# Kernel optimization log

Measured on AMD Instinct MI355X. Metric: run time of the kernel, lower is better.

## Reference

```python
import jax, jax.numpy as jnp
import numpy as np

H = 4096  # grid height
W = 4096  # grid width


def setup_inputs() -> dict:
    key = jax.random.key(0)
    k1, k2 = jax.random.split(key)
    x = jax.random.normal(k1, (H,), dtype=jnp.float32)
    # xavier_uniform with fan_in=3, fan_out=3 => bound = sqrt(6/(3+3)) = 1.0
    bound = float(np.sqrt(6.0 / (3.0 + 3.0)))
    w = jax.random.uniform(k2, (H, W), dtype=jnp.float32, minval=-bound, maxval=bound)
    b = jnp.zeros((H, W), dtype=jnp.float32)
    return {"x": x, "w": w, "b": b}


def _shift_down(a, k):
    # prepend k zero rows / elements along axis 0, drop last k
    pad_shape = (k,) + a.shape[1:]
    return jnp.concatenate([jnp.zeros(pad_shape, a.dtype), a[: a.shape[0] - k]], axis=0)


def reference(x, w, b):
    # The torch module zero-pads w (one row top/bottom) and keeps activation
    # rows 0 and H+1 at zero. The 3-tap stencil a[i-1],a[i],a[i+1] (padded idx)
    # for output row i reduces, in unpadded coords, to:
    #   z[i] = c[i-2]*w[i-2] + c[i-1]*w[i-1] + c[i]*w[i] + b[i]
    # with zero boundary for negative indices.
    Hh, Ww = b.shape
    wm2 = _shift_down(w, 2)  # w[i-2] with zero boundary, (H, W)
    wm1 = _shift_down(w, 1)  # w[i-1]
    # scan across columns (width); carry the activation column (H,)
    xs = (wm2.T, wm1.T, w.T, b.T)  # each (W, H)

    def step(col, ws):
        a2, a1, a0, bj = ws
        z = _shift_down(col, 2) * a2 + _shift_down(col, 1) * a1 + col * a0 + bj
        new = jnp.sin(z)
        return new, None

    final, _ = jax.lax.scan(step, x.reshape(Hh), xs)
    return final.reshape(1, Hh)
```

## Files before the change

### kernel.cpp

```cpp
#include <hip/hip_runtime.h>
#include <math.h>

#define HH 4096
#define WW 4096
#define NB 64
#define U 8
#define NGR (WW / U)
#define GATE 36


__device__ __forceinline__ float f4c(const float4& v, int k) {
    return (k == 0) ? v.x : ((k == 1) ? v.y : ((k == 2) ? v.z : v.w));
}

__device__ __forceinline__ float wave_shr1(float src, float fill) {
    return __int_as_float(__builtin_amdgcn_update_dpp(
        __float_as_int(fill), __float_as_int(src), 0x138, 0xF, 0xF, false));
}

__device__ __forceinline__ float fast_sin(float z) {
    return __builtin_amdgcn_sinf(z * 0.15915494309189535f);
}

#define COLSTEP(COL, M, K)                                                   \
    do {                                                                     \
        float am1 = wave_shr1(a, Hhi[M][K]);                                 \
        float am2 = wave_shr1(am1, Hlo[M][K]);                               \
        const float z = fmaf(am2, f4c(W2v[M][(K) >> 2], (K) & 3),            \
                        fmaf(am1, f4c(W1v[M][(K) >> 2], (K) & 3),            \
                        fmaf(a,   f4c(Wv[M][(K) >> 2],  (K) & 3),            \
                                  f4c(Bv[M][(K) >> 2],  (K) & 3))));         \
        a = fast_sin(z);                                                     \
        if (lane >= 62 && (COL) + 1 < WW) {                                  \
            unsigned long long v =                                           \
                ((unsigned long long)(unsigned)((COL) + 2) << 32) |          \
                (unsigned long long)__float_as_uint(a);                      \
            atomicExch(&hme[(size_t)((COL) + 1) * 2 + (lane - 62)], v);      \
        }                                                                    \
    } while (0)

#define LOADW(M, J)                                                          \
    do {                                                                     \
        const int _j = (J);                                                  \
        Wv[M][0]  = *(const float4*)(wp  + _j);                              \
        Wv[M][1]  = *(const float4*)(wp  + _j + 4);                          \
        W1v[M][0] = *(const float4*)(wp1 + _j);                              \
        W1v[M][1] = *(const float4*)(wp1 + _j + 4);                          \
        W2v[M][0] = *(const float4*)(wp2 + _j);                              \
        W2v[M][1] = *(const float4*)(wp2 + _j + 4);                          \
        Bv[M][0]  = *(const float4*)(bp  + _j);                              \
        Bv[M][1]  = *(const float4*)(bp  + _j + 4);                          \
    } while (0)

#define UNPACKG(GIDX, BUF, SLOT)                                             \
    do {                                                                     \
        const int _jn = (GIDX) * U;                                          \
        if (blk > 0) {                                                       \
            bool myok = (lane >= 16) ||                                      \
                ((unsigned)(Hg[SLOT] >> 32) ==                               \
                 (unsigned)(_jn + (lane >> 1) + 1));                         \
            while (__builtin_expect(!__all(myok), 0)) {                      \
                __builtin_amdgcn_s_sleep(16);                                \
                if (lane < 16)                                               \
                    Hg[SLOT] = atomicOr(&hsrc[(size_t)_jn * 2 + lane], 0ULL);\
                myok = (lane >= 16) ||                                       \
                    ((unsigned)(Hg[SLOT] >> 32) ==                           \
                     (unsigned)(_jn + (lane >> 1) + 1));                     \
            }                                                                \
            float _hv = __uint_as_float((unsigned)(Hg[SLOT] & 0xffffffffu)); \
            _Pragma("unroll")                                                \
            for (int k = 0; k < U; ++k) {                                    \
                Hlo[BUF][k] = __shfl(_hv, 2 * k);                            \
                Hhi[BUF][k] = __shfl(_hv, 2 * k + 1);                        \
            }                                                                \
        }                                                                    \
    } while (0)

#define GROUPBODY(S)                                                         \
    do {                                                                     \
        const int G  = g4 * 4 + (S);                                         \
        const int jb = G * U;                                                \
        if (G + 1 < NGR) UNPACKG(G + 1, ((S) + 1) & 1, ((S) + 1) & 3);       \
        _Pragma("unroll")                                                    \
        for (int k = 0; k < U; ++k) COLSTEP(jb + k, (S) & 1, k);             \
        const int jw = jb + 2 * U;                                           \
        if (jw < WW) LOADW((S) & 1, jw);                                     \
        const int jh = jb + 4 * U;                                           \
        if (jh < WW && blk > 0 && lane < 16)                                 \
            Hg[S] = atomicOr(&hsrc[(size_t)jh * 2 + lane], 0ULL);            \
    } while (0)

__global__ __launch_bounds__(64, 1) void neural_grid_scan(
    const float* __restrict__ x, const float* __restrict__ w,
    const float* __restrict__ bb, float* __restrict__ out,
    unsigned long long* __restrict__ halo)
{
    const int lane = threadIdx.x;
    const int blk  = blockIdx.x;
    const int row  = blk * 64 + lane;
    const int r1 = (row >= 1) ? row - 1 : 0;
    const int r2 = (row >= 2) ? row - 2 : 0;

    const float* wp  = w  + (size_t)row * WW;
    const float* wp1 = w  + (size_t)r1  * WW;
    const float* wp2 = w  + (size_t)r2  * WW;
    const float* bp  = bb + (size_t)row * WW;

    unsigned long long* hme  = halo + (size_t)blk * WW * 2;
    unsigned long long* hsrc = halo + (size_t)(blk - 1) * WW * 2;

    float a = x[row];

    if (lane >= 62) {
        unsigned long long v = (1ULL << 32) | (unsigned long long)__float_as_uint(a);
        atomicExch(&hme[lane - 62], v);
    }

    if (blk > 0 && lane == 0) {
        while ((unsigned)(atomicOr(&hsrc[(size_t)GATE * 2], 0ULL) >> 32)
               != (unsigned)(GATE + 1)) {
            __builtin_amdgcn_s_sleep(8);
        }
    }

    float4 Wv[2][2], W1v[2][2], W2v[2][2], Bv[2][2];
    unsigned long long Hg[4];
    float Hlo[2][U] = {}, Hhi[2][U] = {};

    LOADW(0, 0);
    LOADW(1, U);
    if (blk > 0 && lane < 16) {
        Hg[0] = atomicOr(&hsrc[(size_t)(0 * U) * 2 + lane], 0ULL);
        Hg[1] = atomicOr(&hsrc[(size_t)(1 * U) * 2 + lane], 0ULL);
        Hg[2] = atomicOr(&hsrc[(size_t)(2 * U) * 2 + lane], 0ULL);
        Hg[3] = atomicOr(&hsrc[(size_t)(3 * U) * 2 + lane], 0ULL);
    } else {
        Hg[0] = Hg[1] = Hg[2] = Hg[3] = 0;
    }
    UNPACKG(0, 0, 0);

    for (int g4 = 0; g4 < NGR / 4; ++g4) {
        GROUPBODY(0);
        GROUPBODY(1);
        GROUPBODY(2);
        GROUPBODY(3);
    }

    out[row] = a;
}

extern "C" void kernel_launch(void* const* d_in, const int* in_sizes, int n_in,
                              void* d_out, int out_size, void* d_ws, size_t ws_size,
                              hipStream_t stream) {
    const float* x = (const float*)d_in[0];
    const float* w = (const float*)d_in[1];
    const float* b = (const float*)d_in[2];
    float* out = (float*)d_out;
    unsigned long long* halo = (unsigned long long*)d_ws;
    neural_grid_scan<<<dim3(NB), dim3(64), 0, stream>>>(x, w, b, out, halo);
}
```

Baseline: 904.2 us.

## Process four rows per lane to cut block count and halo chain depth

Each lane now owns four consecutive rows instead of one, so only 16 wavefronts cover the grid instead of 64. This shortens the block-to-block halo dependency chain, and each lane reuses its shared weight rows across its four outputs. In exchange each lane computes four sines per column and loads more weight and bias vectors per group, which raises register pressure and per-wave serial work. The spin-wait sleep is shortened and the start gate is pushed further out.

```diff
diff --git a/kernel.cpp b/kernel.cpp
--- a/kernel.cpp
+++ b/kernel.cpp
@@ -3,10 +3,11 @@
 
 #define HH 4096
 #define WW 4096
-#define NB 64
+#define R 4
+#define NBLK 16
 #define U 8
 #define NGR (WW / U)
-#define GATE 36
+#define GATE 64
 
 
 __device__ __forceinline__ float f4c(const float4& v, int k) {
@@ -24,32 +25,56 @@
 
 #define COLSTEP(COL, M, K)                                                   \
     do {                                                                     \
-        float am1 = wave_shr1(a, Hhi[M][K]);                                 \
-        float am2 = wave_shr1(am1, Hlo[M][K]);                               \
-        const float z = fmaf(am2, f4c(W2v[M][(K) >> 2], (K) & 3),            \
-                        fmaf(am1, f4c(W1v[M][(K) >> 2], (K) & 3),            \
-                        fmaf(a,   f4c(Wv[M][(K) >> 2],  (K) & 3),            \
-                                  f4c(Bv[M][(K) >> 2],  (K) & 3))));         \
-        a = fast_sin(z);                                                     \
-        if (lane >= 62 && (COL) + 1 < WW) {                                  \
-            unsigned long long v =                                           \
-                ((unsigned long long)(unsigned)((COL) + 2) << 32) |          \
-                (unsigned long long)__float_as_uint(a);                      \
-            atomicExch(&hme[(size_t)((COL) + 1) * 2 + (lane - 62)], v);      \
+        const float d1 = wave_shr1(a3, Hhi[M][K]);                           \
+        const float d2 = wave_shr1(a2, Hlo[M][K]);                           \
+        const float w0v = f4c(Wr[M][0][(K) >> 2], (K) & 3);                  \
+        const float w1v = f4c(Wr[M][1][(K) >> 2], (K) & 3);                  \
+        const float w2v = f4c(Wr[M][2][(K) >> 2], (K) & 3);                  \
+        const float w3v = f4c(Wr[M][3][(K) >> 2], (K) & 3);                  \
+        const float w4v = f4c(Wr[M][4][(K) >> 2], (K) & 3);                  \
+        const float w5v = f4c(Wr[M][5][(K) >> 2], (K) & 3);                  \
+        const float n0 = fast_sin(fmaf(d2, w0v, fmaf(d1, w1v,               \
+                          fmaf(a0, w2v, f4c(Br[M][0][(K) >> 2], (K) & 3))))); \
+        const float n1 = fast_sin(fmaf(d1, w1v, fmaf(a0, w2v,               \
+                          fmaf(a1, w3v, f4c(Br[M][1][(K) >> 2], (K) & 3))))); \
+        const float n2 = fast_sin(fmaf(a0, w2v, fmaf(a1, w3v,               \
+                          fmaf(a2, w4v, f4c(Br[M][2][(K) >> 2], (K) & 3))))); \
+        const float n3 = fast_sin(fmaf(a1, w3v, fmaf(a2, w4v,               \
+                          fmaf(a3, w5v, f4c(Br[M][3][(K) >> 2], (K) & 3))))); \
+        a0 = n0; a1 = n1; a2 = n2; a3 = n3;                                  \
+        if (lane == 63 && (COL) + 1 < WW) {                                  \
+            const unsigned long long tg =                                    \
+                ((unsigned long long)(unsigned)((COL) + 2) << 32);           \
+            atomicExch(&hme[(size_t)((COL) + 1) * 2 + 0],                    \
+                       tg | (unsigned long long)__float_as_uint(a2));        \
+            atomicExch(&hme[(size_t)((COL) + 1) * 2 + 1],                    \
+                       tg | (unsigned long long)__float_as_uint(a3));        \
         }                                                                    \
     } while (0)
 
 #define LOADW(M, J)                                                          \
     do {                                                                     \
         const int _j = (J);                                                  \
-        Wv[M][0]  = *(const float4*)(wp  + _j);                              \
-        Wv[M][1]  = *(const float4*)(wp  + _j + 4);                          \
-        W1v[M][0] = *(const float4*)(wp1 + _j);                              \
-        W1v[M][1] = *(const float4*)(wp1 + _j + 4);                          \
-        W2v[M][0] = *(const float4*)(wp2 + _j);                              \
-        W2v[M][1] = *(const float4*)(wp2 + _j + 4);                          \
-        Bv[M][0]  = *(const float4*)(bp  + _j);                              \
-        Bv[M][1]  = *(const float4*)(bp  + _j + 4);                          \
+        Wr[M][0][0] = *(const float4*)(wr0 + _j);                            \
+        Wr[M][0][1] = *(const float4*)(wr0 + _j + 4);                        \
+        Wr[M][1][0] = *(const float4*)(wr1 + _j);                            \
+        Wr[M][1][1] = *(const float4*)(wr1 + _j + 4);                        \
+        Wr[M][2][0] = *(const float4*)(wr2 + _j);                            \
+        Wr[M][2][1] = *(const float4*)(wr2 + _j + 4);                        \
+        Wr[M][3][0] = *(const float4*)(wr3 + _j);                            \
+        Wr[M][3][1] = *(const float4*)(wr3 + _j + 4);                        \
+        Wr[M][4][0] = *(const float4*)(wr4 + _j);                            \
+        Wr[M][4][1] = *(const float4*)(wr4 + _j + 4);                        \
+        Wr[M][5][0] = *(const float4*)(wr5 + _j);                            \
+        Wr[M][5][1] = *(const float4*)(wr5 + _j + 4);                        \
+        Br[M][0][0] = *(const float4*)(br0 + _j);                            \
+        Br[M][0][1] = *(const float4*)(br0 + _j + 4);                        \
+        Br[M][1][0] = *(const float4*)(br1 + _j);                            \
+        Br[M][1][1] = *(const float4*)(br1 + _j + 4);                        \
+        Br[M][2][0] = *(const float4*)(br2 + _j);                            \
+        Br[M][2][1] = *(const float4*)(br2 + _j + 4);                        \
+        Br[M][3][0] = *(const float4*)(br3 + _j);                            \
+        Br[M][3][1] = *(const float4*)(br3 + _j + 4);                        \
     } while (0)
 
 #define UNPACKG(GIDX, BUF, SLOT)                                             \
@@ -60,7 +85,7 @@
                 ((unsigned)(Hg[SLOT] >> 32) ==                               \
                  (unsigned)(_jn + (lane >> 1) + 1));                         \
             while (__builtin_expect(!__all(myok), 0)) {                      \
-                __builtin_amdgcn_s_sleep(16);                                \
+                __builtin_amdgcn_s_sleep(2);                                 \
                 if (lane < 16)                                               \
                     Hg[SLOT] = atomicOr(&hsrc[(size_t)_jn * 2 + lane], 0ULL);\
                 myok = (lane >= 16) ||                                       \
@@ -97,23 +122,28 @@
 {
     const int lane = threadIdx.x;
     const int blk  = blockIdx.x;
-    const int row  = blk * 64 + lane;
-    const int r1 = (row >= 1) ? row - 1 : 0;
-    const int r2 = (row >= 2) ? row - 2 : 0;
+    const int rb   = blk * (64 * R) + lane * R;
 
-    const float* wp  = w  + (size_t)row * WW;
-    const float* wp1 = w  + (size_t)r1  * WW;
-    const float* wp2 = w  + (size_t)r2  * WW;
-    const float* bp  = bb + (size_t)row * WW;
+    const float* wr0 = w + (size_t)((rb >= 2) ? rb - 2 : 0) * WW;
+    const float* wr1 = w + (size_t)((rb >= 1) ? rb - 1 : 0) * WW;
+    const float* wr2 = w + (size_t)rb * WW;
+    const float* wr3 = w + (size_t)(rb + 1) * WW;
+    const float* wr4 = w + (size_t)(rb + 2) * WW;
+    const float* wr5 = w + (size_t)(rb + 3) * WW;
+    const float* br0 = bb + (size_t)rb * WW;
+    const float* br1 = bb + (size_t)(rb + 1) * WW;
+    const float* br2 = bb + (size_t)(rb + 2) * WW;
+    const float* br3 = bb + (size_t)(rb + 3) * WW;
 
     unsigned long long* hme  = halo + (size_t)blk * WW * 2;
     unsigned long long* hsrc = halo + (size_t)(blk - 1) * WW * 2;
 
-    float a = x[row];
+    float4 xv = *(const float4*)(x + rb);
+    float a0 = xv.x, a1 = xv.y, a2 = xv.z, a3 = xv.w;
 
-    if (lane >= 62) {
-        unsigned long long v = (1ULL << 32) | (unsigned long long)__float_as_uint(a);
-        atomicExch(&hme[lane - 62], v);
+    if (lane == 63) {
+        atomicExch(&hme[0], (1ULL << 32) | (unsigned long long)__float_as_uint(a2));
+        atomicExch(&hme[1], (1ULL << 32) | (unsigned long long)__float_as_uint(a3));
     }
 
     if (blk > 0 && lane == 0) {
@@ -123,7 +153,7 @@
         }
     }
 
-    float4 Wv[2][2], W1v[2][2], W2v[2][2], Bv[2][2];
+    float4 Wr[2][6][2], Br[2][4][2];
     unsigned long long Hg[4];
     float Hlo[2][U] = {}, Hhi[2][U] = {};
 
@@ -146,7 +176,7 @@
         GROUPBODY(3);
     }
 
-    out[row] = a;
+    *(float4*)(out + rb) = make_float4(a0, a1, a2, a3);
 }
 
 extern "C" void kernel_launch(void* const* d_in, const int* in_sizes, int n_in,
@@ -157,5 +187,5 @@
     const float* b = (const float*)d_in[2];
     float* out = (float*)d_out;
     unsigned long long* halo = (unsigned long long*)d_ws;
-    neural_grid_scan<<<dim3(NB), dim3(64), 0, stream>>>(x, w, b, out, halo);
+    neural_grid_scan<<<dim3(NBLK), dim3(64), 0, stream>>>(x, w, b, out, halo);
 }
```

After: 1.194 ms. 32.1% more time.

## Offload inter-block halo exchange to a dedicated proxy wavefront via LDS rings

Applied to the files above, without the earlier changes.

Adds a second wavefront per block that takes over all global-memory halo traffic. It publishes this block's boundary values from an LDS output ring to global memory with atomics, and prefetches the upstream block's halo into an LDS input ring. The compute wavefront now only reads and writes LDS with tags, and throttles on a done counter so the output ring does not overflow. The weight prefetch distance grows to four groups (more registers) and the start gate moves to column 48. This is meant to take global atomic latency off the serial column chain, at the cost of proxy polling overhead and an extra LDS hop of latency between blocks.

```diff
diff --git a/kernel.cpp b/kernel.cpp
--- a/kernel.cpp
+++ b/kernel.cpp
@@ -6,7 +6,9 @@
 #define NB 64
 #define U 8
 #define NGR (WW / U)
-#define GATE 36
+#define GATE 48
+#define ORING 256
+#define IRING 128
 
 
 __device__ __forceinline__ float f4c(const float4& v, int k) {
@@ -22,52 +24,50 @@
     return __builtin_amdgcn_sinf(z * 0.15915494309189535f);
 }
 
-#define COLSTEP(COL, M, K)                                                   \
+#define COLSTEP(COL, M, WB, K)                                               \
     do {                                                                     \
         float am1 = wave_shr1(a, Hhi[M][K]);                                 \
         float am2 = wave_shr1(am1, Hlo[M][K]);                               \
-        const float z = fmaf(am2, f4c(W2v[M][(K) >> 2], (K) & 3),            \
-                        fmaf(am1, f4c(W1v[M][(K) >> 2], (K) & 3),            \
-                        fmaf(a,   f4c(Wv[M][(K) >> 2],  (K) & 3),            \
-                                  f4c(Bv[M][(K) >> 2],  (K) & 3))));         \
+        const float z = fmaf(am2, f4c(W2v[WB][(K) >> 2], (K) & 3),           \
+                        fmaf(am1, f4c(W1v[WB][(K) >> 2], (K) & 3),           \
+                        fmaf(a,   f4c(Wv[WB][(K) >> 2],  (K) & 3),           \
+                                  f4c(Bv[WB][(K) >> 2],  (K) & 3))));        \
         a = fast_sin(z);                                                     \
         if (lane >= 62 && (COL) + 1 < WW) {                                  \
-            unsigned long long v =                                           \
-                ((unsigned long long)(unsigned)((COL) + 2) << 32) |          \
-                (unsigned long long)__float_as_uint(a);                      \
-            atomicExch(&hme[(size_t)((COL) + 1) * 2 + (lane - 62)], v);      \
+            const int _oi = ((((COL) + 1) & (ORING - 1)) << 1) + (lane - 62);\
+            vOutVal[_oi] = __float_as_uint(a);              \
+            vOutTag[_oi] = (unsigned)((COL) + 2);\
         }                                                                    \
     } while (0)
 
-#define LOADW(M, J)                                                          \
+#define LOADW(WB, J)                                                         \
     do {                                                                     \
         const int _j = (J);                                                  \
-        Wv[M][0]  = *(const float4*)(wp  + _j);                              \
-        Wv[M][1]  = *(const float4*)(wp  + _j + 4);                          \
-        W1v[M][0] = *(const float4*)(wp1 + _j);                              \
-        W1v[M][1] = *(const float4*)(wp1 + _j + 4);                          \
-        W2v[M][0] = *(const float4*)(wp2 + _j);                              \
-        W2v[M][1] = *(const float4*)(wp2 + _j + 4);                          \
-        Bv[M][0]  = *(const float4*)(bp  + _j);                              \
-        Bv[M][1]  = *(const float4*)(bp  + _j + 4);                          \
-    } while (0)
-
-#define UNPACKG(GIDX, BUF, SLOT)                                             \
-    do {                                                                     \
-        const int _jn = (GIDX) * U;                                          \
+        Wv[WB][0]  = *(const float4*)(wp  + _j);                             \
+        Wv[WB][1]  = *(const float4*)(wp  + _j + 4);                         \
+        W1v[WB][0] = *(const float4*)(wp1 + _j);                             \
+        W1v[WB][1] = *(const float4*)(wp1 + _j + 4);                         \
+        W2v[WB][0] = *(const float4*)(wp2 + _j);                             \
+        W2v[WB][1] = *(const float4*)(wp2 + _j + 4);                         \
+        Bv[WB][0]  = *(const float4*)(bp  + _j);                             \
+        Bv[WB][1]  = *(const float4*)(bp  + _j + 4);                         \
+    } while (0)
+
+#define UNPACKG(GIDX, BUF)                                                   \
+    do {                                                                     \
         if (blk > 0) {                                                       \
-            bool myok = (lane >= 16) ||                                      \
-                ((unsigned)(Hg[SLOT] >> 32) ==                               \
-                 (unsigned)(_jn + (lane >> 1) + 1));                         \
-            while (__builtin_expect(!__all(myok), 0)) {                      \
-                __builtin_amdgcn_s_sleep(16);                                \
-                if (lane < 16)                                               \
-                    Hg[SLOT] = atomicOr(&hsrc[(size_t)_jn * 2 + lane], 0ULL);\
-                myok = (lane >= 16) ||                                       \
-                    ((unsigned)(Hg[SLOT] >> 32) ==                           \
-                     (unsigned)(_jn + (lane >> 1) + 1));                     \
+            const int _col = (GIDX) * U + (lane >> 1);                       \
+            const int _ii  = ((_col & (IRING - 1)) << 1) + (lane & 1);       \
+            unsigned _tag = 0;                                               \
+            for (;;) {                                                       \
+                if (lane < 16) _tag = vInTag[_ii];                           \
+                bool _ok = (lane >= 16) || (_tag == (unsigned)(_col + 1));   \
+                if (__all(_ok)) break;                                       \
+                __builtin_amdgcn_s_sleep(1);                                 \
             }                                                                \
-            float _hv = __uint_as_float((unsigned)(Hg[SLOT] & 0xffffffffu)); \
+            unsigned _val = 0;                                               \
+            if (lane < 16) _val = vInVal[_ii];                               \
+            float _hv = __uint_as_float(_val);                               \
             _Pragma("unroll")                                                \
             for (int k = 0; k < U; ++k) {                                    \
                 Hlo[BUF][k] = __shfl(_hv, 2 * k);                            \
@@ -80,24 +80,89 @@
     do {                                                                     \
         const int G  = g4 * 4 + (S);                                         \
         const int jb = G * U;                                                \
-        if (G + 1 < NGR) UNPACKG(G + 1, ((S) + 1) & 1, ((S) + 1) & 3);       \
+        if (G + 1 < NGR) UNPACKG(G + 1, ((S) + 1) & 1);                      \
         _Pragma("unroll")                                                    \
-        for (int k = 0; k < U; ++k) COLSTEP(jb + k, (S) & 1, k);             \
-        const int jw = jb + 2 * U;                                           \
-        if (jw < WW) LOADW((S) & 1, jw);                                     \
-        const int jh = jb + 4 * U;                                           \
-        if (jh < WW && blk > 0 && lane < 16)                                 \
-            Hg[S] = atomicOr(&hsrc[(size_t)jh * 2 + lane], 0ULL);            \
-    } while (0)
-
-__global__ __launch_bounds__(64, 1) void neural_grid_scan(
+        for (int k = 0; k < U; ++k) COLSTEP(jb + k, (S) & 1, S, k);          \
+        const int jw = jb + 4 * U;                                           \
+        if (jw < WW) LOADW(S, jw);                                           \
+        \
+        \
+        unsigned _done = vOutDone[0];                                        \
+        while (__builtin_expect((int)(jb + 2 * U) > (int)_done + (ORING - 8),\
+                                0)) {                                        \
+            __builtin_amdgcn_s_sleep(4);                                     \
+            _done = vOutDone[0];                                             \
+        }                                                                    \
+    } while (0)
+
+__global__ __launch_bounds__(128, 1) void neural_grid_scan(
     const float* __restrict__ x, const float* __restrict__ w,
     const float* __restrict__ bb, float* __restrict__ out,
     unsigned long long* __restrict__ halo)
 {
-    const int lane = threadIdx.x;
+    __shared__ unsigned ldsOutVal[ORING * 2];
+    __shared__ unsigned ldsOutTag[ORING * 2];
+    __shared__ unsigned ldsInVal[IRING * 2];
+    __shared__ unsigned ldsInTag[IRING * 2];
+    __shared__ unsigned ldsOutDone[1];
+
+    volatile unsigned* vOutVal = ldsOutVal;
+    volatile unsigned* vOutTag = ldsOutTag;
+    volatile unsigned* vInVal  = ldsInVal;
+    volatile unsigned* vInTag  = ldsInTag;
+    volatile unsigned* vOutDone = ldsOutDone;
+
+    const int wv   = threadIdx.x >> 6;
+    const int lane = threadIdx.x & 63;
     const int blk  = blockIdx.x;
-    const int row  = blk * 64 + lane;
+
+    for (int i = threadIdx.x; i < ORING * 2; i += 128) ldsOutTag[i] = 0;
+    for (int i = threadIdx.x; i < IRING * 2; i += 128) ldsInTag[i] = 0;
+    if (threadIdx.x == 0) ldsOutDone[0] = 0;
+    __syncthreads();
+
+    unsigned long long* hme  = halo + (size_t)blk * WW * 2;
+    unsigned long long* hsrc = halo + (size_t)(blk - 1) * WW * 2;
+
+    if (wv == 1) {
+        int cO = 0;
+        int cI = (blk > 0) ? 0 : WW;
+        const int colOfs = lane >> 1;
+        const int slot   = lane & 1;
+        while (cO < WW || cI < WW) {
+            bool prog = false;
+            if (cO < WW) {
+                const int col = cO + colOfs;
+                const int oi  = ((col & (ORING - 1)) << 1) + slot;
+                unsigned tag = vOutTag[oi];
+                if (__all(tag == (unsigned)(col + 1))) {
+                    unsigned val = vOutVal[oi];
+                    atomicExch(&hme[(size_t)col * 2 + slot],
+                               ((unsigned long long)tag << 32) |
+                               (unsigned long long)val);
+                    cO += 32;
+                    if (lane == 0) vOutDone[0] = (unsigned)cO;
+                    prog = true;
+                }
+            }
+            if (cI < WW && cI < cO + 96) {
+                const int col = cI + colOfs;
+                unsigned long long got =
+                    atomicOr(&hsrc[(size_t)col * 2 + slot], 0ULL);
+                if (__all((unsigned)(got >> 32) == (unsigned)(col + 1))) {
+                    const int ii = ((col & (IRING - 1)) << 1) + slot;
+                    vInVal[ii] = (unsigned)(got & 0xffffffffu);
+                    vInTag[ii] = (unsigned)(got >> 32);
+                    cI += 32;
+                    prog = true;
+                }
+            }
+            if (!prog) __builtin_amdgcn_s_sleep(2);
+        }
+        return;
+    }
+
+    const int row = blk * 64 + lane;
     const int r1 = (row >= 1) ? row - 1 : 0;
     const int r2 = (row >= 2) ? row - 2 : 0;
 
@@ -106,14 +171,11 @@
     const float* wp2 = w  + (size_t)r2  * WW;
     const float* bp  = bb + (size_t)row * WW;
 
-    unsigned long long* hme  = halo + (size_t)blk * WW * 2;
-    unsigned long long* hsrc = halo + (size_t)(blk - 1) * WW * 2;
-
     float a = x[row];
 
     if (lane >= 62) {
-        unsigned long long v = (1ULL << 32) | (unsigned long long)__float_as_uint(a);
-        atomicExch(&hme[lane - 62], v);
+        vOutVal[lane - 62] = __float_as_uint(a);
+        vOutTag[lane - 62] = 1u;
     }
 
     if (blk > 0 && lane == 0) {
@@ -123,21 +185,14 @@
         }
     }
 
-    float4 Wv[2][2], W1v[2][2], W2v[2][2], Bv[2][2];
-    unsigned long long Hg[4];
+    float4 Wv[4][2], W1v[4][2], W2v[4][2], Bv[4][2];
     float Hlo[2][U] = {}, Hhi[2][U] = {};
 
     LOADW(0, 0);
     LOADW(1, U);
-    if (blk > 0 && lane < 16) {
-        Hg[0] = atomicOr(&hsrc[(size_t)(0 * U) * 2 + lane], 0ULL);
-        Hg[1] = atomicOr(&hsrc[(size_t)(1 * U) * 2 + lane], 0ULL);
-        Hg[2] = atomicOr(&hsrc[(size_t)(2 * U) * 2 + lane], 0ULL);
-        Hg[3] = atomicOr(&hsrc[(size_t)(3 * U) * 2 + lane], 0ULL);
-    } else {
-        Hg[0] = Hg[1] = Hg[2] = Hg[3] = 0;
-    }
-    UNPACKG(0, 0, 0);
+    LOADW(2, 2 * U);
+    LOADW(3, 3 * U);
+    UNPACKG(0, 0);
 
     for (int g4 = 0; g4 < NGR / 4; ++g4) {
         GROUPBODY(0);
@@ -157,5 +212,5 @@
     const float* b = (const float*)d_in[2];
     float* out = (float*)d_out;
     unsigned long long* halo = (unsigned long long*)d_ws;
-    neural_grid_scan<<<dim3(NB), dim3(64), 0, stream>>>(x, w, b, out, halo);
-}
+    neural_grid_scan<<<dim3(NB), dim3(128), 0, stream>>>(x, w, b, out, halo);
+}
```

After: 1.745 ms. +93.0%, slower.
